# Kernel tuning notes

Hardware: AMD Instinct MI355X
Metric: run time of the kernel (lower is better)

Reference implementation:

```python
import jax, jax.numpy as jnp
import numpy as np

N = 50000      # nodes
E = 1600000    # edges
F_IN = 8       # node_features
H = 64         # hidden_dim
P = 5          # poly_degree
L = 3          # n_layers


def setup_inputs() -> dict:
    key = jax.random.key(0)
    ks = jax.random.split(key, 20)
    s = lambda *shape: 0.05
    inp = {
        "x": jax.random.normal(ks[0], (N, F_IN), jnp.float32),
        "edge_index": jax.random.randint(ks[1], (2, E), 0, N, jnp.int32),
        "edge_weight": jax.random.uniform(ks[2], (E,), jnp.float32),
        # input projection (xavier-ish)
        "W_in": jax.random.normal(ks[3], (H, F_IN), jnp.float32) * 0.15,
        "b_in": jnp.zeros((H,), jnp.float32),
        # per-layer coeff_net: Linear(H+4 -> 32) -> ReLU -> Linear(32 -> P+1) -> Softmax
        "coeff_W1": jax.random.normal(ks[4], (L, 32, H + 4), jnp.float32) * 0.1,
        "coeff_b1": jnp.zeros((L, 32), jnp.float32),
        "coeff_W2": jax.random.normal(ks[5], (L, P + 1, 32), jnp.float32) * 0.1,
        "coeff_b2": jnp.zeros((L, P + 1), jnp.float32),
        # per-layer LayerNorm params
        "ln_scale": jnp.ones((L, H), jnp.float32),
        "ln_bias": jnp.zeros((L, H), jnp.float32),
        # edge predictor: Linear(2H->H) ReLU Linear(H->H//2) ReLU Linear(H//2->1) Sigmoid
        "ep_W1": jax.random.normal(ks[6], (H, 2 * H), jnp.float32) * 0.08,
        "ep_b1": jnp.zeros((H,), jnp.float32),
        "ep_W2": jax.random.normal(ks[7], (H // 2, H), jnp.float32) * 0.1,
        "ep_b2": jnp.zeros((H // 2,), jnp.float32),
        "ep_W3": jax.random.normal(ks[8], (1, H // 2), jnp.float32) * 0.15,
        "ep_b3": jnp.zeros((1,), jnp.float32),
    }
    return inp


def _layernorm(v, scale, bias, eps=1e-5):
    m = v.mean(-1, keepdims=True)
    var = v.var(-1, keepdims=True)
    return (v - m) / jnp.sqrt(var + eps) * scale + bias


def _diffusion(h, row, col, norm, cW1, cb1, cW2, cb2):
    # coefficient MLP conditioned on graph stats (std is unbiased, as torch)
    x_mean = h.mean(0)
    stats = jnp.stack([h.mean(), h.std(ddof=1),
                       jnp.float32(N), jnp.float32(E)])
    ci = jnp.concatenate([x_mean, stats])           # (H+4,)
    hid = jax.nn.relu(ci @ cW1.T + cb1)             # (32,)
    coeffs = jax.nn.softmax(hid @ cW2.T + cb2)      # (P+1,)
    result = coeffs[0] * h
    tx = h
    for k in range(1, P + 1):
        msg = norm[:, None] * tx[col]               # (E, H) gather + scale
        tx = jax.ops.segment_sum(msg, row, num_segments=N)  # scatter-add SpMM
        result = result + coeffs[k] * tx
    return result


def reference(x, edge_index, edge_weight,
              W_in, b_in,
              coeff_W1, coeff_b1, coeff_W2, coeff_b2,
              ln_scale, ln_bias,
              ep_W1, ep_b1, ep_W2, ep_b2, ep_W3, ep_b3):
    row, col = edge_index[0], edge_index[1]
    # symmetric normalization T = D^{-1/2} A D^{-1/2} (identical every layer)
    deg = jnp.zeros((N,), x.dtype).at[col].add(edge_weight)
    dis = jnp.minimum(deg ** -0.5, 1e6)             # clamp(max=1e6) caps inf
    dis = jnp.where(jnp.isinf(dis), 0.0, dis)
    norm = dis[row] * edge_weight * dis[col]        # (E,)

    h = x @ W_in.T + b_in                           # (N, H)
    for l in range(L):
        h_new = _diffusion(h, row, col, norm,
                           coeff_W1[l], coeff_b1[l], coeff_W2[l], coeff_b2[l])
        h = _layernorm(h + h_new, ln_scale[l], ln_bias[l])

    ef = jnp.concatenate([h[row], h[col]], axis=-1)             # (E, 2H)
    e1 = jax.nn.relu(ef @ ep_W1.T + ep_b1)
    e2 = jax.nn.relu(e1 @ ep_W2.T + ep_b2)
    edge_preds = jax.nn.sigmoid(e2 @ ep_W3.T + ep_b3)[:, 0]     # (E,)
    return edge_preds, h
```

## Files before the change

### kernel.cpp

```cpp
#include <hip/hip_runtime.h>
#include <hip/hip_bf16.h>
#include <hip/hip_fp16.h>

typedef __hip_bfloat16 bf16;
typedef __attribute__((ext_vector_type(8))) short short8;
typedef __attribute__((ext_vector_type(8))) _Float16 half8;
typedef __attribute__((ext_vector_type(2))) _Float16 half2v;
typedef __attribute__((ext_vector_type(4))) float f32x4;

#define N_NODES 50000
#define N_EDGES 1600000
#define FIN 8
#define HD 64
#define NH (N_NODES * HD)
#define NLAYERS 3

#define RSLC 256
#define EPR (N_EDGES / RSLC)
#define NWORDS 12500

__device__ __forceinline__ float b2f(bf16 v) { return __bfloat162float(v); }
__device__ __forceinline__ float bu2f(unsigned int u) { return __uint_as_float(u << 16); }
__device__ __forceinline__ unsigned short f2bu(float f) {
    unsigned int x = __float_as_uint(f);
    unsigned int r = x + 0x7FFFu + ((x >> 16) & 1u);
    return (unsigned short)(r >> 16);
}
__device__ __forceinline__ unsigned short f2h(float f) {
    _Float16 h = (_Float16)f;
    return *(unsigned short*)&h;
}
union H16 { unsigned short b; _Float16 h; };
__device__ __forceinline__ float h16f(unsigned u) {
    H16 x; x.b = (unsigned short)u;
    return (float)x.h;
}

__global__ void k_detect(const void* __restrict__ ew, int* __restrict__ flag) {
    int ok = 1;
    for (int i = threadIdx.x; i < 512; i += 64) {
        float v = b2f(((const bf16*)ew)[i]);
        if (!(v >= 0.f && v <= 1.f)) ok = 0;
    }
    unsigned long long m = __ballot(ok);
    if (threadIdx.x == 0) *flag = (m == 0xFFFFFFFFFFFFFFFFull) ? 0 : 1;
}

struct ConvArgs {
    const void* src[14];
    float* dst[14];
    int cum[15];
};

__global__ void k_conv_small(ConvArgs a, const int* __restrict__ flag) {
    int q = blockIdx.x * 256 + threadIdx.x;
    if (q >= a.cum[14]) return;
    int s = 0;
    while (q >= a.cum[s + 1]) ++s;
    int off = q - a.cum[s];
    if (*flag) a.dst[s][off] = ((const float*)a.src[s])[off];
    else       a.dst[s][off] = bu2f(((const unsigned short*)a.src[s])[off]);
}

__global__ void k_deg(const int* __restrict__ ei, const void* __restrict__ ewr,
                      const int* __restrict__ flag, float* __restrict__ deg) {
    int e = blockIdx.x * 256 + threadIdx.x;
    if (e >= N_EDGES) return;
    int c = ei[N_EDGES + e];
    float w = (*flag) ? ((const float*)ewr)[e] : bu2f(((const unsigned short*)ewr)[e]);
    atomicAdd(&deg[c], w);
}


__global__ void __launch_bounds__(256) k_hist_row(const int* __restrict__ ei,
                                                  unsigned int* __restrict__ pcnt_u32) {
    __shared__ unsigned int sm[NWORDS];
    int b = blockIdx.x, t = threadIdx.x;
    for (int i = t; i < NWORDS; i += 256) sm[i] = 0;
    __syncthreads();
    int ebase = b * EPR;
    for (int el = t; el < EPR; el += 256) {
        int r = ei[ebase + el];
        atomicAdd(&sm[r >> 2], 1u << ((r & 3) * 8));
    }
    __syncthreads();
    unsigned int* dst = pcnt_u32 + (size_t)b * NWORDS;
    for (int i = t; i < NWORDS; i += 256) dst[i] = sm[i];
}

__global__ void k_merge(const unsigned char* __restrict__ pcnt8,
                        const float* __restrict__ deg,
                        int* __restrict__ cnt, float* __restrict__ dis,
                        float* __restrict__ dis2,
                        unsigned short* __restrict__ pref16, int* __restrict__ bsum) {
    __shared__ int red[256];
    int t = threadIdx.x;
    int n = blockIdx.x * 256 + t;
    int run = 0;
    if (n < N_NODES) {
#pragma unroll 8
        for (int s = 0; s < RSLC; ++s) {
            pref16[(size_t)s * N_NODES + n] = (unsigned short)run;
            run += pcnt8[(size_t)s * N_NODES + n];
        }
        cnt[n] = run;
        float di = fminf(rsqrtf(deg[n]), 1e6f);
        dis[n] = di;
        dis2[n] = di * di;
    }
    red[t] = run;
    __syncthreads();
    for (int off = 128; off; off >>= 1) {
        if (t < off) red[t] += red[t + off];
        __syncthreads();
    }
    if (t == 0) bsum[blockIdx.x] = red[0];
}

__global__ void k_scan_top(const int* __restrict__ bsum, int* __restrict__ bpre,
                           int* __restrict__ row_ptr) {
    __shared__ int sm[256];
    int t = threadIdx.x;
    int v = (t < 196) ? bsum[t] : 0;
    sm[t] = v;
    __syncthreads();
    int val = v;
    for (int off = 1; off < 256; off <<= 1) {
        int other = (t >= off) ? sm[t - off] : 0;
        __syncthreads();
        val += other;
        sm[t] = val;
        __syncthreads();
    }
    bpre[t] = val - v;
    if (t == 0) row_ptr[N_NODES] = N_EDGES;
}

__global__ void k_scan_fin(const int* __restrict__ cnt, const int* __restrict__ bpre,
                           int* __restrict__ row_ptr) {
    __shared__ int sm[256];
    int t = threadIdx.x;
    int n = blockIdx.x * 256 + t;
    int v = (n < N_NODES) ? cnt[n] : 0;
    sm[t] = v;
    __syncthreads();
    int val = v;
    for (int off = 1; off < 256; off <<= 1) {
        int other = (t >= off) ? sm[t - off] : 0;
        __syncthreads();
        val += other;
        sm[t] = val;
        __syncthreads();
    }
    if (n < N_NODES) row_ptr[n] = bpre[blockIdx.x] + val - v;
}

__global__ void __launch_bounds__(256) k_placeA(const int* __restrict__ ei,
                                                const void* __restrict__ ewr,
                                                const int* __restrict__ flag,
                                                const int* __restrict__ row_ptr,
                                                const unsigned short* __restrict__ pref16,
                                                unsigned int* __restrict__ pairs4,
                                                int* __restrict__ iperm) {
    __shared__ unsigned int sm[NWORDS];
    int b = blockIdx.x, t = threadIdx.x;
    for (int i = t; i < NWORDS; i += 256) sm[i] = 0;
    __syncthreads();
    int f32 = *flag;
    int ebase = b * EPR;
    const unsigned short* pr = pref16 + (size_t)b * N_NODES;
    for (int el = t; el < EPR; el += 256) {
        int e = ebase + el;
        int r = ei[e];
        int c = ei[N_EDGES + e];
        float w = f32 ? ((const float*)ewr)[e] : bu2f(((const unsigned short*)ewr)[e]);
        int sh = (r & 3) * 8;
        unsigned old = atomicAdd(&sm[r >> 2], 1u << sh);
        int ord = (old >> sh) & 0xFF;
        int pos = row_ptr[r] + pr[r] + ord;
        pairs4[pos] = ((unsigned)c << 16) | (unsigned)f2h(w);
        iperm[e] = pos;
    }
}

__global__ void __launch_bounds__(256) k_rc(const int* __restrict__ row_ptr,
                                            const unsigned int* __restrict__ pairs4,
                                            unsigned int* __restrict__ rc) {
    int lane = threadIdx.x & 63;
    int wv = __builtin_amdgcn_readfirstlane((int)(blockIdx.x * 4 + (threadIdx.x >> 6)));
    int s = __builtin_amdgcn_readfirstlane(row_ptr[wv]);
    int e = __builtin_amdgcn_readfirstlane(row_ptr[wv + 1]);
    unsigned rhi = ((unsigned)wv) << 16;
    for (int pos = s + lane; pos < e; pos += 64)
        rc[pos] = (pairs4[pos] >> 16) | rhi;
}


__global__ void k_inproj(const void* __restrict__ xr_, const float* __restrict__ W,
                         const float* __restrict__ b, const float* __restrict__ dis,
                         float* __restrict__ h,
                         unsigned short* __restrict__ h_bf, const int* __restrict__ flag) {
    __shared__ float Wt[FIN * HD];
    __shared__ float bs[HD];
    int t = threadIdx.x;
    int f32 = *flag;
    for (int idx = t; idx < FIN * HD; idx += 256) {
        int f = idx >> 3, j = idx & 7;
        Wt[j * 64 + f] = W[idx];
    }
    if (t < 64) bs[t] = b[t];
    __syncthreads();
    int gid = blockIdx.x * 256 + t;
    if (gid < NH) {
        int i = gid >> 6, f = gid & 63;
        const float* xf = (const float*)xr_ + i * FIN;
        const unsigned short* xb = (const unsigned short*)xr_ + i * FIN;
        float acc = bs[f];
#pragma unroll
        for (int j = 0; j < FIN; ++j) {
            float xv = f32 ? xf[j] : bu2f(xb[j]);
            acc += xv * Wt[j * 64 + f];
        }
        h[gid] = acc;
        h_bf[gid] = f2bu(acc * dis[i]);
    }
}


__global__ void k_stats(const float* __restrict__ h, float* __restrict__ stats) {
    __shared__ float ssum[256], ssq[256];
    int t = threadIdx.x;
    float ls = 0.f, lq = 0.f;
    for (int idx = blockIdx.x * 256 + t; idx < NH; idx += 102400) {
        float v = h[idx];
        ls += v; lq += v * v;
    }
    ssum[t] = ls; ssq[t] = lq;
    __syncthreads();
    if (t < 64) {
        float a = ssum[t] + ssum[t + 64] + ssum[t + 128] + ssum[t + 192];
        atomicAdd(&stats[t], a);
        float q = ssq[t] + ssq[t + 64] + ssq[t + 128] + ssq[t + 192];
        for (int off = 32; off; off >>= 1) q += __shfl_down(q, off, 64);
        if (t == 0) atomicAdd(&stats[64], q);
    }
}

__global__ void k_coeffs(const float* __restrict__ stats,
                         const float* __restrict__ W1, const float* __restrict__ b1,
                         const float* __restrict__ W2, const float* __restrict__ b2,
                         int layer, float* __restrict__ coeffs) {
    __shared__ float ci[68];
    __shared__ float hid[32];
    __shared__ float lg[6];
    int t = threadIdx.x;
    float sf = stats[t];
    float tot = sf;
    for (int off = 1; off < 64; off <<= 1) tot += __shfl_xor(tot, off, 64);
    ci[t] = sf / (float)N_NODES;
    if (t == 0) {
        float sumsq = stats[64];
        float mean = tot / (float)NH;
        float var = (sumsq - (float)NH * mean * mean) / (float)(NH - 1);
        ci[64] = mean;
        ci[65] = sqrtf(fmaxf(var, 0.f));
        ci[66] = (float)N_NODES;
        ci[67] = (float)N_EDGES;
    }
    __syncthreads();
    if (t < 32) {
        float a = b1[layer * 32 + t];
        const float* wr = W1 + (layer * 32 + t) * 68;
        for (int j = 0; j < 68; ++j) a += ci[j] * wr[j];
        hid[t] = fmaxf(a, 0.f);
    }
    __syncthreads();
    if (t < 6) {
        float a = b2[layer * 6 + t];
        const float* wr = W2 + (layer * 6 + t) * 32;
        for (int g = 0; g < 32; ++g) a += hid[g] * wr[g];
        lg[t] = a;
    }
    __syncthreads();
    if (t == 0) {
        float mx = lg[0];
        for (int p = 1; p < 6; ++p) mx = fmaxf(mx, lg[p]);
        float s = 0.f, e[6];
        for (int p = 0; p < 6; ++p) { e[p] = expf(lg[p] - mx); s += e[p]; }
        for (int p = 0; p < 6; ++p) coeffs[p] = e[p] / s;
    }
}


__device__ __forceinline__ float acc_range(const unsigned short* __restrict__ txo,
                                           const unsigned int* __restrict__ pairs4,
                                           int j0, int j1, int lane, float acc) {
    int j = j0;
    for (; j + 15 < j1; j += 16) {
        unsigned p0 = pairs4[j],      p1 = pairs4[j + 1],  p2 = pairs4[j + 2],  p3 = pairs4[j + 3];
        unsigned p4 = pairs4[j + 4],  p5 = pairs4[j + 5],  p6 = pairs4[j + 6],  p7 = pairs4[j + 7];
        unsigned p8 = pairs4[j + 8],  p9 = pairs4[j + 9],  pa = pairs4[j + 10], pb = pairs4[j + 11];
        unsigned pc = pairs4[j + 12], pd = pairs4[j + 13], pe = pairs4[j + 14], pf = pairs4[j + 15];
        float g0 = bu2f(txo[(p0 >> 16) * 64 + lane]);
        float g1 = bu2f(txo[(p1 >> 16) * 64 + lane]);
        float g2 = bu2f(txo[(p2 >> 16) * 64 + lane]);
        float g3 = bu2f(txo[(p3 >> 16) * 64 + lane]);
        float g4 = bu2f(txo[(p4 >> 16) * 64 + lane]);
        float g5 = bu2f(txo[(p5 >> 16) * 64 + lane]);
        float g6 = bu2f(txo[(p6 >> 16) * 64 + lane]);
        float g7 = bu2f(txo[(p7 >> 16) * 64 + lane]);
        float g8 = bu2f(txo[(p8 >> 16) * 64 + lane]);
        float g9 = bu2f(txo[(p9 >> 16) * 64 + lane]);
        float ga = bu2f(txo[(pa >> 16) * 64 + lane]);
        float gb = bu2f(txo[(pb >> 16) * 64 + lane]);
        float gc = bu2f(txo[(pc >> 16) * 64 + lane]);
        float gd = bu2f(txo[(pd >> 16) * 64 + lane]);
        float ge = bu2f(txo[(pe >> 16) * 64 + lane]);
        float gf = bu2f(txo[(pf >> 16) * 64 + lane]);
        acc += h16f(p0) * g0 + h16f(p1) * g1 + h16f(p2) * g2 + h16f(p3) * g3;
        acc += h16f(p4) * g4 + h16f(p5) * g5 + h16f(p6) * g6 + h16f(p7) * g7;
        acc += h16f(p8) * g8 + h16f(p9) * g9 + h16f(pa) * ga + h16f(pb) * gb;
        acc += h16f(pc) * gc + h16f(pd) * gd + h16f(pe) * ge + h16f(pf) * gf;
    }
    for (; j + 7 < j1; j += 8) {
        unsigned p0 = pairs4[j],     p1 = pairs4[j + 1], p2 = pairs4[j + 2], p3 = pairs4[j + 3];
        unsigned p4 = pairs4[j + 4], p5 = pairs4[j + 5], p6 = pairs4[j + 6], p7 = pairs4[j + 7];
        float g0 = bu2f(txo[(p0 >> 16) * 64 + lane]);
        float g1 = bu2f(txo[(p1 >> 16) * 64 + lane]);
        float g2 = bu2f(txo[(p2 >> 16) * 64 + lane]);
        float g3 = bu2f(txo[(p3 >> 16) * 64 + lane]);
        float g4 = bu2f(txo[(p4 >> 16) * 64 + lane]);
        float g5 = bu2f(txo[(p5 >> 16) * 64 + lane]);
        float g6 = bu2f(txo[(p6 >> 16) * 64 + lane]);
        float g7 = bu2f(txo[(p7 >> 16) * 64 + lane]);
        acc += h16f(p0) * g0 + h16f(p1) * g1 + h16f(p2) * g2 + h16f(p3) * g3;
        acc += h16f(p4) * g4 + h16f(p5) * g5 + h16f(p6) * g6 + h16f(p7) * g7;
    }
    for (; j < j1; ++j) {
        unsigned p = pairs4[j];
        acc += h16f(p) * bu2f(txo[(p >> 16) * 64 + lane]);
    }
    return acc;
}

__global__ void __launch_bounds__(256) k_spmm(
    const unsigned short* __restrict__ txo, unsigned short* __restrict__ txn,
    const int* __restrict__ row_ptr, const unsigned int* __restrict__ pairs4,
    const float* __restrict__ dis2) {
    int lane = threadIdx.x & 63;
    int wv = __builtin_amdgcn_readfirstlane((int)(blockIdx.x * 4 + (threadIdx.x >> 6)));
    int s = __builtin_amdgcn_readfirstlane(row_ptr[wv]);
    int e = __builtin_amdgcn_readfirstlane(row_ptr[wv + 1]);
    float acc = acc_range(txo, pairs4, s, e, lane, 0.f);
    float d2 = dis2[wv];
    txn[wv * 64 + lane] = f2bu(acc * d2);
}


__global__ void __launch_bounds__(256) k_spmm_ln(
    const unsigned short* __restrict__ txo,
    const int* __restrict__ row_ptr, const unsigned int* __restrict__ pairs4,
    float* __restrict__ h, unsigned short* __restrict__ h_bf,
    const unsigned short* __restrict__ t1, const unsigned short* __restrict__ t2,
    const unsigned short* __restrict__ t3, const unsigned short* __restrict__ t4,
    const float* __restrict__ coeffs, const float* __restrict__ dis,
    const float* __restrict__ sc, const float* __restrict__ bi,
    int layer, int last, void* __restrict__ outv, const int* __restrict__ flag) {
    int lane = threadIdx.x & 63;
    int wv = __builtin_amdgcn_readfirstlane((int)(blockIdx.x * 4 + (threadIdx.x >> 6)));
    int s = __builtin_amdgcn_readfirstlane(row_ptr[wv]);
    int e = __builtin_amdgcn_readfirstlane(row_ptr[wv + 1]);
    float acc = acc_range(txo, pairs4, s, e, lane, 0.f);
    int o = wv * 64 + lane;
    float ds = dis[wv];
    float invd = 1.f / ds;
    float c0 = coeffs[0], c1 = coeffs[1], c2 = coeffs[2],
          c3 = coeffs[3], c4 = coeffs[4], c5 = coeffs[5];
    float v = (1.f + c0) * h[o] +
              invd * (c1 * bu2f(t1[o]) + c2 * bu2f(t2[o]) +
                      c3 * bu2f(t3[o]) + c4 * bu2f(t4[o])) +
              c5 * ds * acc;
    float m = v;
    for (int off = 1; off < 64; off <<= 1) m += __shfl_xor(m, off, 64);
    m *= (1.f / 64.f);
    float d = v - m;
    float q = d * d;
    for (int off = 1; off < 64; off <<= 1) q += __shfl_xor(q, off, 64);
    float var = q * (1.f / 64.f);
    float y = d / sqrtf(var + 1e-5f) * sc[layer * 64 + lane] + bi[layer * 64 + lane];
    h[o] = y;
    h_bf[o] = f2bu(y * ds);
    if (last) {
        if (*flag) ((float*)outv)[N_EDGES + o] = y;
        else       ((unsigned short*)outv)[N_EDGES + o] = f2bu(y);
    }
}


__global__ void __launch_bounds__(256) k_uv(const float* __restrict__ h,
                                            const float* __restrict__ W1,
                                            unsigned short* __restrict__ ub,
                                            unsigned short* __restrict__ vb) {
    __shared__ float Wt[128 * 65];
    __shared__ float hs[4 * 64];
    int t = threadIdx.x;
    for (int idx = t; idx < 8192; idx += 256) {
        int f = idx >> 7, j = idx & 127;
        Wt[j * 65 + f] = W1[idx];
    }
    int node0 = blockIdx.x * 4;
    hs[t] = h[node0 * 64 + t];
    __syncthreads();
    int ni = t >> 6, f = t & 63;
    const float* hr = hs + ni * 64;
    float au = 0.f, av = 0.f;
#pragma unroll 8
    for (int j = 0; j < 64; ++j) {
        float xv = hr[j];
        au += Wt[j * 65 + f] * xv;
        av += Wt[(j + 64) * 65 + f] * xv;
    }
    int i = node0 + ni;
    ub[i * 64 + f] = f2h(au);
    vb[i * 64 + f] = f2h(av);
}

__device__ __forceinline__ unsigned h2rel(unsigned uu, unsigned vv, half2v b) {
    half2v a = *(half2v*)&uu + *(half2v*)&vv + b;
    a[0] = a[0] > (_Float16)0 ? a[0] : (_Float16)0;
    a[1] = a[1] > (_Float16)0 ? a[1] : (_Float16)0;
    return *(unsigned*)&a;
}

union U4H8 { uint4 u; half8 h; };

__global__ void __launch_bounds__(256) k_edgepred(
    const unsigned short* __restrict__ ub, const unsigned short* __restrict__ vb,
    const unsigned int* __restrict__ rc,
    const float* __restrict__ eb1, const float* __restrict__ eW2,
    const float* __restrict__ eb2, const float* __restrict__ eW3,
    const float* __restrict__ eb3, float* __restrict__ tmpP) {
    int t = threadIdx.x;
    int lane = t & 63;
    int m = lane & 15, q = lane >> 4;

    half8 B00, B01, B10, B11;
#pragma unroll
    for (int j = 0; j < 8; ++j) {
        B00[j] = (_Float16)eW2[(m) * 64      + q * 8 + j];
        B01[j] = (_Float16)eW2[(m) * 64 + 32 + q * 8 + j];
        B10[j] = (_Float16)eW2[(m + 16) * 64      + q * 8 + j];
        B11[j] = (_Float16)eW2[(m + 16) * 64 + 32 + q * 8 + j];
    }
    half2v b1p0[4], b1p1[4];
#pragma unroll
    for (int wq = 0; wq < 4; ++wq) {
        b1p0[wq][0] = (_Float16)eb1[q * 8 + 2 * wq];
        b1p0[wq][1] = (_Float16)eb1[q * 8 + 2 * wq + 1];
        b1p1[wq][0] = (_Float16)eb1[32 + q * 8 + 2 * wq];
        b1p1[wq][1] = (_Float16)eb1[32 + q * 8 + 2 * wq + 1];
    }
    float w3a = eW3[m], w3b = eW3[16 + m];
    float b2a = eb2[m], b2b = eb2[16 + m];
    float b3v = eb3[0];

    int gw = blockIdx.x * 4 + (t >> 6);
    const int NW = 1563 * 4;
    for (int tile = gw; tile < N_EDGES / 16; tile += NW) {
        int base = tile << 4;
        unsigned rcv = rc[base + m];
        int col = rcv & 0xFFFF;
        int row = rcv >> 16;
        const unsigned short* up = ub + row * 64;
        const unsigned short* vp = vb + col * 64;
        uint4 U0 = *(const uint4*)(up + q * 8);
        uint4 U1 = *(const uint4*)(up + 32 + q * 8);
        uint4 V0 = *(const uint4*)(vp + q * 8);
        uint4 V1 = *(const uint4*)(vp + 32 + q * 8);
        U4H8 a0, a1;
        a0.u.x = h2rel(U0.x, V0.x, b1p0[0]);
        a0.u.y = h2rel(U0.y, V0.y, b1p0[1]);
        a0.u.z = h2rel(U0.z, V0.z, b1p0[2]);
        a0.u.w = h2rel(U0.w, V0.w, b1p0[3]);
        a1.u.x = h2rel(U1.x, V1.x, b1p1[0]);
        a1.u.y = h2rel(U1.y, V1.y, b1p1[1]);
        a1.u.z = h2rel(U1.z, V1.z, b1p1[2]);
        a1.u.w = h2rel(U1.w, V1.w, b1p1[3]);
        f32x4 acc0 = {0.f, 0.f, 0.f, 0.f};
        f32x4 acc1 = {0.f, 0.f, 0.f, 0.f};
        acc0 = __builtin_amdgcn_mfma_f32_16x16x32_f16(a0.h, B00, acc0, 0, 0, 0);
        acc0 = __builtin_amdgcn_mfma_f32_16x16x32_f16(a1.h, B01, acc0, 0, 0, 0);
        acc1 = __builtin_amdgcn_mfma_f32_16x16x32_f16(a0.h, B10, acc1, 0, 0, 0);
        acc1 = __builtin_amdgcn_mfma_f32_16x16x32_f16(a1.h, B11, acc1, 0, 0, 0);
        float z[4];
#pragma unroll
        for (int rr = 0; rr < 4; ++rr) {
            z[rr] = w3a * fmaxf(acc0[rr] + b2a, 0.f) + w3b * fmaxf(acc1[rr] + b2b, 0.f);
            z[rr] += __shfl_xor(z[rr], 1, 64);
            z[rr] += __shfl_xor(z[rr], 2, 64);
            z[rr] += __shfl_xor(z[rr], 4, 64);
            z[rr] += __shfl_xor(z[rr], 8, 64);
        }
        if (m == 0) {
#pragma unroll
            for (int rr = 0; rr < 4; ++rr) {
                float p = 1.f / (1.f + __expf(-(z[rr] + b3v)));
                tmpP[base + (q << 2) + rr] = p;
            }
        }
    }
}

__global__ void k_out(const int* __restrict__ iperm, const float* __restrict__ tmpP,
                      void* __restrict__ outv, const int* __restrict__ flag) {
    int e = blockIdx.x * 256 + threadIdx.x;
    if (e >= N_EDGES) return;
    float p = tmpP[iperm[e]];
    if (*flag) ((float*)outv)[e] = p;
    else       ((unsigned short*)outv)[e] = f2bu(p);
}


extern "C" void kernel_launch(void* const* d_in, const int* in_sizes, int n_in,
                              void* d_out, int out_size, void* d_ws, size_t ws_size,
                              hipStream_t stream) {
    (void)in_sizes; (void)n_in; (void)out_size; (void)ws_size;
    const void* x_r   = d_in[0];
    const int*  ei    = (const int*)d_in[1];
    const void* ew_r  = d_in[2];

    char* w = (char*)d_ws;
    float* h            = (float*)w;          w += (size_t)NH * 4;
    unsigned short* hbf = (unsigned short*)w; w += (size_t)NH * 2;
    char* txr           = w;                  w += (size_t)NH * 8;
    unsigned int* pairs4 = (unsigned int*)w;  w += (size_t)N_EDGES * 4;
    unsigned int* rc    = (unsigned int*)w;   w += (size_t)N_EDGES * 4;
    int* iperm          = (int*)w;            w += (size_t)N_EDGES * 4;
    int* row_ptr        = (int*)w;            w += 200192;
    int* cnt            = (int*)w;            w += 200192;
    float* dis          = (float*)w;          w += 200192;
    float* dis2         = (float*)w;          w += 200192;
    float* cWin = (float*)w; w += 2048;
    float* cbin = (float*)w; w += 256;
    float* ccW1 = (float*)w; w += 26112;
    float* ccb1 = (float*)w; w += 384;
    float* ccW2 = (float*)w; w += 2304;
    float* ccb2 = (float*)w; w += 128;
    float* clns = (float*)w; w += 768;
    float* clnb = (float*)w; w += 768;
    float* ceW1 = (float*)w; w += 32768;
    float* ceb1 = (float*)w; w += 256;
    float* ceW2 = (float*)w; w += 8192;
    float* ceb2 = (float*)w; w += 128;
    float* ceW3 = (float*)w; w += 128;
    float* ceb3 = (float*)w; w += 128;
    int* bsum = (int*)w; w += 1024;
    int* bpre = (int*)w; w += 1024;
    char* zero_base = w;
    float* stats = (float*)w; w += 1024;
    float* deg   = (float*)w; w += 200192;
    size_t zero_bytes = (size_t)(w - zero_base);
    float* coeffs = (float*)w; w += 128;
    int*   flag   = (int*)w;   w += 128;

    unsigned int* pcnt_u32 = (unsigned int*)pairs4;
    unsigned char* pcnt8   = (unsigned char*)pairs4;
    unsigned short* pref16 = (unsigned short*)txr;
    float* tmpP            = (float*)pairs4;

    unsigned short* tx[4];
    for (int k = 0; k < 4; ++k) tx[k] = (unsigned short*)txr + (size_t)k * NH;
    unsigned short* ub = tx[0];
    unsigned short* vb = tx[1];

    (void)hipMemsetAsync(zero_base, 0, zero_bytes, stream);

    k_detect<<<1, 64, 0, stream>>>(ew_r, flag);

    ConvArgs ca;
    const void* srcs[14] = {d_in[3], d_in[4], d_in[5], d_in[6], d_in[7], d_in[8], d_in[9],
                            d_in[10], d_in[11], d_in[12], d_in[13], d_in[14], d_in[15], d_in[16]};
    float* dsts[14] = {cWin, cbin, ccW1, ccb1, ccW2, ccb2, clns,
                       clnb, ceW1, ceb1, ceW2, ceb2, ceW3, ceb3};
    int sizes[14] = {512, 64, 6528, 96, 576, 18, 192, 192, 8192, 64, 2048, 32, 32, 1};
    int c = 0;
    for (int i = 0; i < 14; ++i) { ca.src[i] = srcs[i]; ca.dst[i] = dsts[i]; ca.cum[i] = c; c += sizes[i]; }
    ca.cum[14] = c;
    k_conv_small<<<(c + 255) / 256, 256, 0, stream>>>(ca, flag);

    k_deg<<<6250, 256, 0, stream>>>(ei, ew_r, flag, deg);
    k_hist_row<<<RSLC, 256, 0, stream>>>(ei, pcnt_u32);
    k_merge<<<196, 256, 0, stream>>>(pcnt8, deg, cnt, dis, dis2, pref16, bsum);
    k_scan_top<<<1, 256, 0, stream>>>(bsum, bpre, row_ptr);
    k_scan_fin<<<196, 256, 0, stream>>>(cnt, bpre, row_ptr);
    k_placeA<<<RSLC, 256, 0, stream>>>(ei, ew_r, flag, row_ptr, pref16, pairs4, iperm);
    k_rc<<<12500, 256, 0, stream>>>(row_ptr, pairs4, rc);
    k_inproj<<<12500, 256, 0, stream>>>(x_r, cWin, cbin, dis, h, hbf, flag);

    for (int l = 0; l < NLAYERS; ++l) {
        k_stats<<<400, 256, 0, stream>>>(h, stats + l * 80);
        k_coeffs<<<1, 64, 0, stream>>>(stats + l * 80, ccW1, ccb1, ccW2, ccb2, l,
                                       coeffs + l * 8);
        const unsigned short* src = hbf;
        for (int k = 0; k < 4; ++k) {
            k_spmm<<<12500, 256, 0, stream>>>(src, tx[k], row_ptr, pairs4, dis2);
            src = tx[k];
        }
        k_spmm_ln<<<12500, 256, 0, stream>>>(tx[3], row_ptr, pairs4, h, hbf,
                                             tx[0], tx[1], tx[2], tx[3],
                                             coeffs + l * 8, dis, clns, clnb, l,
                                             (l == NLAYERS - 1) ? 1 : 0, d_out, flag);
    }

    k_uv<<<12500, 256, 0, stream>>>(h, ceW1, ub, vb);
    k_edgepred<<<1563, 256, 0, stream>>>(ub, vb, rc, ceb1, ceW2, ceb2, ceW3, ceb3, tmpP);
    k_out<<<6250, 256, 0, stream>>>(iperm, tmpP, d_out, flag);
}
```

Measured before the change: 921.9 us.

## Split node features into two half-planes for cache-friendlier SpMM gathers

Stores the bf16 node-feature buffers as two planes of 32 features each and launches the SpMM over twice as many blocks, with adjacent blocks taking alternate halves. Each wave splits its lanes into even and odd edge streams and combines them with a cross-lane shuffle. The aim is a smaller gather working set per pass, so the half-feature table stays in L2/MALL, while two edges are processed per wave step. In exchange, the edge list and row pointers are read twice, and the last SpMM writes the full layout so the LN kernel can consume it, which adds layout-mixing complexity.

```diff
diff --git a/kernel.cpp b/kernel.cpp
--- a/kernel.cpp
+++ b/kernel.cpp
@@ -13,6 +13,7 @@
 #define FIN 8
 #define HD 64
 #define NH (N_NODES * HD)
+#define HHALF (N_NODES * 32)
 #define NLAYERS 3
 
 #define RSLC 256
@@ -222,7 +223,7 @@
             acc += xv * Wt[j * 64 + f];
         }
         h[gid] = acc;
-        h_bf[gid] = f2bu(acc * dis[i]);
+        h_bf[(size_t)(f >> 5) * HHALF + i * 32 + (f & 31)] = f2bu(acc * dis[i]);
     }
 }
 
@@ -288,6 +289,82 @@
         float s = 0.f, e[6];
         for (int p = 0; p < 6; ++p) { e[p] = expf(lg[p] - mx); s += e[p]; }
         for (int p = 0; p < 6; ++p) coeffs[p] = e[p] / s;
+    }
+}
+
+
+__device__ __forceinline__ float acc_range_h(const unsigned short* __restrict__ src,
+                                             const unsigned int* __restrict__ pairs4,
+                                             int j0, int j1, int odd, int f, float acc) {
+    int j = j0;
+    for (; j + 15 < j1; j += 16) {
+        unsigned p0 = pairs4[j],      p1 = pairs4[j + 1],  p2 = pairs4[j + 2],  p3 = pairs4[j + 3];
+        unsigned p4 = pairs4[j + 4],  p5 = pairs4[j + 5],  p6 = pairs4[j + 6],  p7 = pairs4[j + 7];
+        unsigned p8 = pairs4[j + 8],  p9 = pairs4[j + 9],  pa = pairs4[j + 10], pb = pairs4[j + 11];
+        unsigned pc = pairs4[j + 12], pd = pairs4[j + 13], pe = pairs4[j + 14], pf = pairs4[j + 15];
+        unsigned q0 = odd ? p1 : p0;
+        unsigned q1 = odd ? p3 : p2;
+        unsigned q2 = odd ? p5 : p4;
+        unsigned q3 = odd ? p7 : p6;
+        unsigned q4 = odd ? p9 : p8;
+        unsigned q5 = odd ? pb : pa;
+        unsigned q6 = odd ? pd : pc;
+        unsigned q7 = odd ? pf : pe;
+        float g0 = bu2f(src[(q0 >> 16) * 32 + f]);
+        float g1 = bu2f(src[(q1 >> 16) * 32 + f]);
+        float g2 = bu2f(src[(q2 >> 16) * 32 + f]);
+        float g3 = bu2f(src[(q3 >> 16) * 32 + f]);
+        float g4 = bu2f(src[(q4 >> 16) * 32 + f]);
+        float g5 = bu2f(src[(q5 >> 16) * 32 + f]);
+        float g6 = bu2f(src[(q6 >> 16) * 32 + f]);
+        float g7 = bu2f(src[(q7 >> 16) * 32 + f]);
+        acc += h16f(q0) * g0 + h16f(q1) * g1 + h16f(q2) * g2 + h16f(q3) * g3;
+        acc += h16f(q4) * g4 + h16f(q5) * g5 + h16f(q6) * g6 + h16f(q7) * g7;
+    }
+    for (; j + 7 < j1; j += 8) {
+        unsigned p0 = pairs4[j],     p1 = pairs4[j + 1], p2 = pairs4[j + 2], p3 = pairs4[j + 3];
+        unsigned p4 = pairs4[j + 4], p5 = pairs4[j + 5], p6 = pairs4[j + 6], p7 = pairs4[j + 7];
+        unsigned q0 = odd ? p1 : p0;
+        unsigned q1 = odd ? p3 : p2;
+        unsigned q2 = odd ? p5 : p4;
+        unsigned q3 = odd ? p7 : p6;
+        float g0 = bu2f(src[(q0 >> 16) * 32 + f]);
+        float g1 = bu2f(src[(q1 >> 16) * 32 + f]);
+        float g2 = bu2f(src[(q2 >> 16) * 32 + f]);
+        float g3 = bu2f(src[(q3 >> 16) * 32 + f]);
+        acc += h16f(q0) * g0 + h16f(q1) * g1 + h16f(q2) * g2 + h16f(q3) * g3;
+    }
+    for (; j + 1 < j1; j += 2) {
+        unsigned p0 = pairs4[j], p1 = pairs4[j + 1];
+        unsigned q = odd ? p1 : p0;
+        acc += h16f(q) * bu2f(src[(q >> 16) * 32 + f]);
+    }
+    if (j < j1) {
+        unsigned p0 = pairs4[j];
+        unsigned q = odd ? 0u : p0;
+        acc += h16f(q) * bu2f(src[(q >> 16) * 32 + f]);
+    }
+    return acc;
+}
+
+__global__ void __launch_bounds__(256) k_spmm(
+    const unsigned short* __restrict__ txo, unsigned short* __restrict__ txn,
+    const int* __restrict__ row_ptr, const unsigned int* __restrict__ pairs4,
+    const float* __restrict__ dis2, int full_out) {
+    int t = threadIdx.x;
+    int lane = t & 63;
+    int f = lane & 31, odd = lane >> 5;
+    int hsel = blockIdx.x & 1;
+    int wv = __builtin_amdgcn_readfirstlane((int)((blockIdx.x >> 1) * 4 + (t >> 6)));
+    const unsigned short* src = txo + (size_t)hsel * HHALF;
+    int s = __builtin_amdgcn_readfirstlane(row_ptr[wv]);
+    int e = __builtin_amdgcn_readfirstlane(row_ptr[wv + 1]);
+    float acc = acc_range_h(src, pairs4, s, e, odd, f, 0.f);
+    acc += __shfl_xor(acc, 32, 64);
+    if (odd == 0) {
+        unsigned short v = f2bu(acc * dis2[wv]);
+        if (full_out) txn[wv * 64 + hsel * 32 + f] = v;
+        else          txn[(size_t)hsel * HHALF + wv * 32 + f] = v;
     }
 }
 
@@ -343,20 +420,6 @@
     return acc;
 }
 
-__global__ void __launch_bounds__(256) k_spmm(
-    const unsigned short* __restrict__ txo, unsigned short* __restrict__ txn,
-    const int* __restrict__ row_ptr, const unsigned int* __restrict__ pairs4,
-    const float* __restrict__ dis2) {
-    int lane = threadIdx.x & 63;
-    int wv = __builtin_amdgcn_readfirstlane((int)(blockIdx.x * 4 + (threadIdx.x >> 6)));
-    int s = __builtin_amdgcn_readfirstlane(row_ptr[wv]);
-    int e = __builtin_amdgcn_readfirstlane(row_ptr[wv + 1]);
-    float acc = acc_range(txo, pairs4, s, e, lane, 0.f);
-    float d2 = dis2[wv];
-    txn[wv * 64 + lane] = f2bu(acc * d2);
-}
-
-
 __global__ void __launch_bounds__(256) k_spmm_ln(
     const unsigned short* __restrict__ txo,
     const int* __restrict__ row_ptr, const unsigned int* __restrict__ pairs4,
@@ -372,13 +435,14 @@
     int e = __builtin_amdgcn_readfirstlane(row_ptr[wv + 1]);
     float acc = acc_range(txo, pairs4, s, e, lane, 0.f);
     int o = wv * 64 + lane;
+    size_t so = (size_t)(lane >> 5) * HHALF + wv * 32 + (lane & 31);
     float ds = dis[wv];
     float invd = 1.f / ds;
     float c0 = coeffs[0], c1 = coeffs[1], c2 = coeffs[2],
           c3 = coeffs[3], c4 = coeffs[4], c5 = coeffs[5];
     float v = (1.f + c0) * h[o] +
-              invd * (c1 * bu2f(t1[o]) + c2 * bu2f(t2[o]) +
-                      c3 * bu2f(t3[o]) + c4 * bu2f(t4[o])) +
+              invd * (c1 * bu2f(t1[so]) + c2 * bu2f(t2[so]) +
+                      c3 * bu2f(t3[so]) + c4 * bu2f(t4[o])) +
               c5 * ds * acc;
     float m = v;
     for (int off = 1; off < 64; off <<= 1) m += __shfl_xor(m, off, 64);
@@ -389,7 +453,7 @@
     float var = q * (1.f / 64.f);
     float y = d / sqrtf(var + 1e-5f) * sc[layer * 64 + lane] + bi[layer * 64 + lane];
     h[o] = y;
-    h_bf[o] = f2bu(y * ds);
+    h_bf[so] = f2bu(y * ds);
     if (last) {
         if (*flag) ((float*)outv)[N_EDGES + o] = y;
         else       ((unsigned short*)outv)[N_EDGES + o] = f2bu(y);
@@ -601,11 +665,10 @@
         k_stats<<<400, 256, 0, stream>>>(h, stats + l * 80);
         k_coeffs<<<1, 64, 0, stream>>>(stats + l * 80, ccW1, ccb1, ccW2, ccb2, l,
                                        coeffs + l * 8);
-        const unsigned short* src = hbf;
-        for (int k = 0; k < 4; ++k) {
-            k_spmm<<<12500, 256, 0, stream>>>(src, tx[k], row_ptr, pairs4, dis2);
-            src = tx[k];
-        }
+        k_spmm<<<25000, 256, 0, stream>>>(hbf,   tx[0], row_ptr, pairs4, dis2, 0);
+        k_spmm<<<25000, 256, 0, stream>>>(tx[0], tx[1], row_ptr, pairs4, dis2, 0);
+        k_spmm<<<25000, 256, 0, stream>>>(tx[1], tx[2], row_ptr, pairs4, dis2, 0);
+        k_spmm<<<25000, 256, 0, stream>>>(tx[2], tx[3], row_ptr, pairs4, dis2, 1);
         k_spmm_ln<<<12500, 256, 0, stream>>>(tx[3], row_ptr, pairs4, h, hbf,
                                              tx[0], tx[1], tx[2], tx[3],
                                              coeffs + l * 8, dis, clns, clnb, l,
```

New measurement: 1.040 ms. 1.13x slower.
